# Optimization experiments

Hardware: AMD Instinct MI355X
Metric: run time of the kernel (lower is better)

The kernel has to match this reference:

```python
import jax, jax.numpy as jnp
import numpy as np
from jax import lax

HEADS = 4
DSTATE = 8
DHALF = 64
DTRANK = 8
GRID_SIZE = 5
SPLINE_ORDER = 3


def _ln(x, g, b, eps=1e-5):
    mu = x.mean(-1, keepdims=True)
    v = ((x - mu) ** 2).mean(-1, keepdims=True)
    return (x - mu) / jnp.sqrt(v + eps) * g + b


def _make_grid(in_f):
    h = 2.0 / GRID_SIZE
    g = jnp.arange(-SPLINE_ORDER, GRID_SIZE + SPLINE_ORDER + 1, dtype=jnp.float32) * h - 1.0
    return jnp.tile(g[None, :], (in_f, 1))  # (in, grid+2k+1)


def _b_splines(x, grid):
    # x: (batch, in); grid: (in, G+2k+1) -> (batch, in, G+k)
    xe = x[:, :, None]
    bases = ((xe >= grid[:, :-1]) & (xe < grid[:, 1:])).astype(x.dtype)
    for k in range(1, SPLINE_ORDER + 1):
        bases = ((xe - grid[:, :-(k + 1)]) / (grid[:, k:-1] - grid[:, :-(k + 1)])) * bases[:, :, :-1] \
              + ((grid[:, k + 1:] - xe) / (grid[:, k + 1:] - grid[:, 1:-k])) * bases[:, :, 1:]
    return bases


def _kan_layer(x, bw, sw, sc, grid):
    base = jax.nn.silu(x) @ bw.T
    bs = _b_splines(x, grid)
    return base + jnp.einsum('bic,oic->bo', bs, sw * sc[:, :, None])


def _fkan(x, ng, nb, bw0, sw0, sc0, bw1, sw1, sc1):
    B, N, C = x.shape
    xf = _ln(x, ng, nb).reshape(B * N, C)
    h = _kan_layer(xf, bw0, sw0, sc0, _make_grid(C))
    y = _kan_layer(h, bw1, sw1, sc1, _make_grid(bw0.shape[0]))
    return y.reshape(B, N, C)


def _conv1x1(x, w, b):
    return jnp.einsum('bchw,oc->bohw', x, w[:, :, 0, 0]) + b[None, :, None, None]


def _dwconv2d(x, w, b):
    y = lax.conv_general_dilated(x, w, (1, 1), 'SAME', feature_group_count=x.shape[1],
                                 dimension_numbers=('NCHW', 'OIHW', 'NCHW'))
    return y + b[None, :, None, None]


def _dwconv1d(x, w):
    return lax.conv_general_dilated(x, w, (1,), 'SAME', feature_group_count=x.shape[1],
                                    dimension_numbers=('NCH', 'OIH', 'NCH'))


def _attention(x, temp, qkv_w, qkv_b, dw_w, dw_b, po_w, po_b):
    b, c, h, w = x.shape
    qkv = _dwconv2d(_conv1x1(x, qkv_w, qkv_b), dw_w, dw_b)
    q, k, v = jnp.split(qkv, 3, axis=1)
    rs = lambda t: t.reshape(b, HEADS, c // HEADS, h * w)
    q, k, v = rs(q), rs(k), rs(v)
    q = q / jnp.maximum(jnp.linalg.norm(q, axis=-1, keepdims=True), 1e-12)
    k = k / jnp.maximum(jnp.linalg.norm(k, axis=-1, keepdims=True), 1e-12)
    attn = jax.nn.softmax(jnp.einsum('bhcn,bhdn->bhcd', q, k) * temp, axis=-1)
    out = jnp.einsum('bhcd,bhdn->bhcn', attn, v).reshape(b, c, h, w)
    return _conv1x1(out, po_w, po_b)


def _mamba(x, in_w, xp_w, dt_w, dt_b, A_log, Dp, out_w, cx_w, cz_w):
    B, L, C = x.shape
    xz = x @ in_w.T                       # (B, L, d_inner)
    xc, zc = jnp.split(xz, 2, axis=-1)    # each (B, L, DHALF)
    xl = jax.nn.silu(_dwconv1d(xc.transpose(0, 2, 1), cx_w)).transpose(0, 2, 1)
    zl = jax.nn.silu(_dwconv1d(zc.transpose(0, 2, 1), cz_w)).transpose(0, 2, 1)
    x_dbl = xl @ xp_w.T                   # (B, L, dt_rank + 2*d_state)
    dt, Bm, Cm = jnp.split(x_dbl, [DTRANK, DTRANK + DSTATE], axis=-1)
    delta = jax.nn.softplus(dt @ dt_w.T + dt_b)   # (B, L, DHALF)
    A = -jnp.exp(A_log)                   # (DHALF, DSTATE)
    dA = jnp.exp(jnp.einsum('bld,dn->bldn', delta, A))
    dBu = delta[..., None] * Bm[:, :, None, :] * xl[..., None]

    def step(hst, inp):
        dA_t, dBu_t, C_t = inp
        hst = dA_t * hst + dBu_t
        return hst, jnp.einsum('bdn,bn->bd', hst, C_t)

    h0 = jnp.zeros((B, DHALF, DSTATE), x.dtype)
    _, ys = lax.scan(step, h0, (dA.transpose(1, 0, 2, 3), dBu.transpose(1, 0, 2, 3), Cm.transpose(1, 0, 2)))
    y = ys.transpose(1, 0, 2) + xl * Dp
    return jnp.concatenate([y, zl], axis=-1) @ out_w.T


def _forward(x5d, ln1_g, ln1_b, ln2_g, ln2_b, ln3_g, ln3_b, ln4_g, ln4_b,
             attn_temp, attn_qkv_w, attn_qkv_b, attn_dw_w, attn_dw_b, attn_po_w, attn_po_b,
             ffn1_ng, ffn1_nb, ffn1_bw0, ffn1_sw0, ffn1_sc0, ffn1_bw1, ffn1_sw1, ffn1_sc1,
             ffn2_ng, ffn2_nb, ffn2_bw0, ffn2_sw0, ffn2_sc0, ffn2_bw1, ffn2_sw1, ffn2_sc1,
             in_proj_w, x_proj_w, dt_proj_w, dt_proj_b, A_log, D_param, out_proj_w, conv_x_w, conv_z_w):
    B, C, Dd, H, W = x5d.shape
    N = Dd * H * W
    Hs = int(np.sqrt(N))
    x = x5d.reshape(B, C, N).transpose(0, 2, 1)   # (B, N, C)
    t2d = _ln(x, ln1_g, ln1_b).transpose(0, 2, 1).reshape(B, C, Hs, Hs)
    a = _attention(t2d, attn_temp, attn_qkv_w, attn_qkv_b, attn_dw_w, attn_dw_b, attn_po_w, attn_po_b)
    t = x + a.reshape(B, C, N).transpose(0, 2, 1)
    u = _fkan(_ln(t, ln2_g, ln2_b), ffn1_ng, ffn1_nb, ffn1_bw0, ffn1_sw0, ffn1_sc0, ffn1_bw1, ffn1_sw1, ffn1_sc1) + t
    x_tr = x + u
    m = _mamba(_ln(x_tr, ln3_g, ln3_b), in_proj_w, x_proj_w, dt_proj_w, dt_proj_b, A_log, D_param, out_proj_w, conv_x_w, conv_z_w) + x_tr
    n = _fkan(_ln(m, ln4_g, ln4_b), ffn2_ng, ffn2_nb, ffn2_bw0, ffn2_sw0, ffn2_sc0, ffn2_bw1, ffn2_sw1, ffn2_sc1) + m
    out = x_tr + n
    return out.transpose(0, 2, 1).reshape(B, C, Dd, H, W)


def setup_inputs():
    key = jax.random.key(0)
    ks = iter(jax.random.split(key, 48))
    f32 = jnp.float32

    def rn(shape, s=0.05):
        return jax.random.normal(next(ks), shape, f32) * s

    B, C, Dd, H, W = 2, 128, 1, 96, 96
    MLP = 512
    d = {}
    d['x5d'] = jax.random.normal(next(ks), (B, C, Dd, H, W), f32)
    for nm in ('ln1', 'ln2', 'ln3', 'ln4'):
        d[nm + '_g'] = jnp.ones((C,), f32)
        d[nm + '_b'] = jnp.zeros((C,), f32)
    d['attn_temp'] = jnp.ones((HEADS, 1, 1), f32)
    d['attn_qkv_w'] = rn((3 * C, C, 1, 1)); d['attn_qkv_b'] = jnp.zeros((3 * C,), f32)
    d['attn_dw_w'] = rn((3 * C, 1, 3, 3), 0.2); d['attn_dw_b'] = jnp.zeros((3 * C,), f32)
    d['attn_po_w'] = rn((C, C, 1, 1)); d['attn_po_b'] = jnp.zeros((C,), f32)
    for p in ('ffn1', 'ffn2'):
        d[p + '_ng'] = jnp.ones((C,), f32); d[p + '_nb'] = jnp.zeros((C,), f32)
        d[p + '_bw0'] = rn((MLP, C)); d[p + '_sw0'] = rn((MLP, C, GRID_SIZE + SPLINE_ORDER), 0.02); d[p + '_sc0'] = jnp.ones((MLP, C), f32)
        d[p + '_bw1'] = rn((C, MLP)); d[p + '_sw1'] = rn((C, MLP, GRID_SIZE + SPLINE_ORDER), 0.02); d[p + '_sc1'] = jnp.ones((C, MLP), f32)
    d['in_proj_w'] = rn((C, C))
    d['x_proj_w'] = rn((DTRANK + 2 * DSTATE, DHALF))
    std = DTRANK ** -0.5
    d['dt_proj_w'] = jax.random.uniform(next(ks), (DHALF, DTRANK), f32, -std, std)
    dt = jnp.exp(jax.random.uniform(next(ks), (DHALF,), f32) * (np.log(0.1) - np.log(0.001)) + np.log(0.001))
    dt = jnp.clip(dt, 1e-4, None)
    d['dt_proj_b'] = dt + jnp.log(-jnp.expm1(-dt))
    d['A_log'] = jnp.log(jnp.tile(jnp.arange(1, DSTATE + 1, dtype=f32)[None, :], (DHALF, 1)))
    d['D_param'] = jnp.ones((DHALF,), f32)
    d['out_proj_w'] = rn((C, C))
    d['conv_x_w'] = rn((DHALF, 1, 3), 0.2)
    d['conv_z_w'] = rn((DHALF, 1, 3), 0.2)
    return d


def reference(x5d, ln1_g, ln1_b, ln2_g, ln2_b, ln3_g, ln3_b, ln4_g, ln4_b,
              attn_temp, attn_qkv_w, attn_qkv_b, attn_dw_w, attn_dw_b, attn_po_w, attn_po_b,
              ffn1_ng, ffn1_nb, ffn1_bw0, ffn1_sw0, ffn1_sc0, ffn1_bw1, ffn1_sw1, ffn1_sc1,
              ffn2_ng, ffn2_nb, ffn2_bw0, ffn2_sw0, ffn2_sc0, ffn2_bw1, ffn2_sw1, ffn2_sc1,
              in_proj_w, x_proj_w, dt_proj_w, dt_proj_b, A_log, D_param, out_proj_w, conv_x_w, conv_z_w):
    return _forward(x5d, ln1_g, ln1_b, ln2_g, ln2_b, ln3_g, ln3_b, ln4_g, ln4_b,
                    attn_temp, attn_qkv_w, attn_qkv_b, attn_dw_w, attn_dw_b, attn_po_w, attn_po_b,
                    ffn1_ng, ffn1_nb, ffn1_bw0, ffn1_sw0, ffn1_sc0, ffn1_bw1, ffn1_sw1, ffn1_sc1,
                    ffn2_ng, ffn2_nb, ffn2_bw0, ffn2_sw0, ffn2_sc0, ffn2_bw1, ffn2_sw1, ffn2_sc1,
                    in_proj_w, x_proj_w, dt_proj_w, dt_proj_b, A_log, D_param, out_proj_w, conv_x_w, conv_z_w)
```

## Files before the change

### kernel.cpp

```cpp
#include <hip/hip_runtime.h>

typedef unsigned short u16;
typedef __attribute__((ext_vector_type(8))) short bh8;
typedef __attribute__((ext_vector_type(4))) float f4;

#define DI __device__ __forceinline__

DI u16 f2bf(float f){ unsigned u=__float_as_uint(f); u += 0x7fffu + ((u>>16)&1u); return (u16)(u>>16); }
DI float bf2f(u16 u){ return __uint_as_float(((unsigned)u)<<16); }
DI float silu_f(float x){ return x/(1.f+__expf(-x)); }

DI void gld16(const u16* g, u16* l){
  __builtin_amdgcn_global_load_lds((const __attribute__((address_space(1))) void*)g,
                                   (__attribute__((address_space(3))) void*)l, 16, 0, 0);
}

DI void bspline8(float x, float* v){
  float u = x*2.5f + 5.5f;
  #pragma unroll
  for (int j=0;j<8;j++){
    float a  = fabsf(u - (float)(j+2));
    float t1 = fmaxf(2.f-a, 0.f);
    float t2 = fmaxf(1.f-a, 0.f);
    v[j] = t1*t1*t1*(1.f/6.f) - t2*t2*t2*(2.f/3.f);
  }
}

template<int KAN_H, bool OUT_BF16>
__global__ __launch_bounds__(256, 4)
void gemm64(const void* __restrict__ Asrc, const u16* __restrict__ Bt,
            void* __restrict__ Cout, int M, int N, int K, int ktiles_per_z,
            int split, const float* __restrict__ bias, const float* __restrict__ R1)
{
  __shared__ u16 sA[64*64 + 8];
  __shared__ u16 sB[128*64];
  const int m0 = blockIdx.y * 64;
  const int n0 = blockIdx.x * 128;
  const int ktiles = K >> 6;
  int kt0 = blockIdx.z * ktiles_per_z;
  int kt1 = kt0 + ktiles_per_z; if (kt1 > ktiles) kt1 = ktiles;
  const int t = threadIdx.x;
  const int wave = t >> 6, lane = t & 63;
  const int lr = lane & 15, lq = lane >> 4;
  const int lr8 = lane >> 3, lc8 = lane & 7;
  const int swz8 = lc8 ^ lr8;
  f4 acc[4][2];
  f4 z4 = {0.f,0.f,0.f,0.f};
  #pragma unroll
  for (int i=0;i<4;i++){ acc[i][0]=z4; acc[i][1]=z4; }

  for (int kt = kt0; kt < kt1; ++kt) {
    int k0 = kt << 6;
    {
      const u16* Bp = Bt + (size_t)n0 * K + k0;
      #pragma unroll
      for (int it=0; it<4; ++it) {
        int r = it*32 + wave*8;
        gld16(Bp + (size_t)(r + lr8) * K + swz8*8, &sB[r*64]);
      }
    }
    if (KAN_H == 0) {
      const u16* Ap = (const u16*)Asrc + (size_t)m0 * K + k0;
      #pragma unroll
      for (int it=0; it<2; ++it) {
        int r = it*32 + wave*8;
        gld16(Ap + (size_t)(r + lr8) * K + swz8*8, &sA[r*64]);
      }
    } else {
      const u16* hsrc = (const u16*)Asrc;
      if (k0 < KAN_H) {
        #pragma unroll
        for (int it=0; it<2; ++it) {
          int chunk = t + it*256;
          int r = chunk >> 3, ck = chunk & 7;
          const u16* src = hsrc + (size_t)(m0+r)*KAN_H + k0 + ck*8;
          ushort4 a = *(const ushort4*)src;
          ushort4 b2 = *(const ushort4*)(src+4);
          alignas(16) u16 o[8];
          o[0]=f2bf(silu_f(bf2f(a.x))); o[1]=f2bf(silu_f(bf2f(a.y)));
          o[2]=f2bf(silu_f(bf2f(a.z))); o[3]=f2bf(silu_f(bf2f(a.w)));
          o[4]=f2bf(silu_f(bf2f(b2.x))); o[5]=f2bf(silu_f(bf2f(b2.y)));
          o[6]=f2bf(silu_f(bf2f(b2.z))); o[7]=f2bf(silu_f(bf2f(b2.w)));
          *(float4*)(&sA[r*64 + (ck ^ (r&7))*8]) = *(const float4*)o;
        }
      } else {
        int i0 = (k0 - KAN_H) >> 3;
        const float4 zf4 = make_float4(0.f,0.f,0.f,0.f);
        #pragma unroll
        for (int it=0; it<2; ++it) {
          int pair = t + it*256;
          int r = pair >> 3, ii = pair & 7;
          int base = r*64 + (ii ^ (r&7))*8;
          *(float4*)(&sA[base]) = zf4;
          float x = bf2f(hsrc[(size_t)(m0+r)*KAN_H + i0 + ii]);
          float u = x*2.5f + 5.5f;
          bool valid = (u >= 0.f) & (u < 11.f);
          float uc = fminf(fmaxf(u, 0.f), 10.999f);
          int m = (int)uc;
          float tt = uc - (float)m;
          float omt = 1.f - tt, t2 = tt*tt, t3 = t2*tt;
          float w0 = omt*omt*omt*(1.f/6.f);
          float w3 = t3*(1.f/6.f);
          float w1 = 0.5f*t3 - t2 + (2.f/3.f);
          float w2 = 1.f - w0 - w1 - w3;
          float ws[4] = {w0, w1, w2, w3};
          int c0 = m - 3;
          #pragma unroll
          for (int j=0;j<4;j++){
            int c = c0 + j;
            bool ok = valid & ((unsigned)c < 8u);
            int off = ok ? (base + c) : (64*64);
            sA[off] = f2bf(ws[j]);
          }
        }
      }
    }
    __syncthreads();
    #pragma unroll
    for (int kk=0; kk<64; kk+=32) {
      const int c0k = kk >> 3;
      bh8 af[4], bfr[2];
      #pragma unroll
      for (int i=0;i<4;i++) {
        int row = i*16 + lr;
        af[i] = *(const bh8*)(&sA[row*64 + ((c0k+lq) ^ (row&7))*8]);
      }
      #pragma unroll
      for (int j=0;j<2;j++) {
        int row = wave*32 + j*16 + lr;
        bfr[j] = *(const bh8*)(&sB[row*64 + ((c0k+lq) ^ (row&7))*8]);
      }
      #pragma unroll
      for (int i=0;i<4;i++)
        #pragma unroll
        for (int j=0;j<2;j++)
          acc[i][j] = __builtin_amdgcn_mfma_f32_16x16x32_bf16(af[i], bfr[j], acc[i][j], 0, 0, 0);
    }
    __syncthreads();
  }
  float* Cf = (float*)Cout;
  if (!OUT_BF16 && split) Cf += (size_t)blockIdx.z * M * N;
  u16* Cb = (u16*)Cout;
  #pragma unroll
  for (int i=0;i<4;i++) {
    int row = m0 + i*16 + lq*4;
    #pragma unroll
    for (int j=0;j<2;j++) {
      int col = n0 + wave*32 + j*16 + lr;
      float bv = bias ? bias[col] : 0.f;
      #pragma unroll
      for (int r4=0;r4<4;r4++) {
        size_t idx = (size_t)(row + r4) * N + col;
        float v = acc[i][j][r4] + bv;
        if (OUT_BF16) {
          Cb[idx] = f2bf(v);
        } else {
          if (R1) v += R1[idx];
          Cf[idx] = v;
        }
      }
    }
  }
}

__global__ __launch_bounds__(256) void k_ln1_trans(const float* __restrict__ x5d,
    float* __restrict__ x_t, u16* __restrict__ ln1_t,
    const float* __restrict__ g, const float* __restrict__ bv)
{
  __shared__ float tile[128*65];
  __shared__ float red_s[256], red_q[256];
  __shared__ float st_mu[64], st_rs[64];
  int b = blockIdx.y, n0 = blockIdx.x * 64;
  int j = threadIdx.x & 63, part = threadIdx.x >> 6;
  for (int cc=0; cc<32; ++cc) {
    int c = part*32 + cc;
    tile[c*65 + j] = x5d[((size_t)b*128 + c)*9216 + n0 + j];
  }
  __syncthreads();
  float s=0.f, s2=0.f;
  for (int cc=0; cc<32; ++cc) {
    float v = tile[(part*32+cc)*65 + j];
    s += v; s2 += v*v;
  }
  red_s[threadIdx.x]=s; red_q[threadIdx.x]=s2;
  __syncthreads();
  if (threadIdx.x < 64) {
    int jj = threadIdx.x;
    float ts = red_s[jj]+red_s[jj+64]+red_s[jj+128]+red_s[jj+192];
    float tq = red_q[jj]+red_q[jj+64]+red_q[jj+128]+red_q[jj+192];
    float mu = ts*(1.f/128.f);
    st_mu[jj]=mu;
    st_rs[jj]=rsqrtf(tq*(1.f/128.f) - mu*mu + 1e-5f);
  }
  __syncthreads();
  for (int it=0; it<32; ++it) {
    int idx = threadIdx.x + it*256;
    int tok = idx >> 7, c = idx & 127;
    float v = tile[c*65 + tok];
    size_t a = ((size_t)b*9216 + n0 + tok)*128 + c;
    x_t[a] = v;
    ln1_t[a] = f2bf((v - st_mu[tok])*st_rs[tok]*g[c] + bv[c]);
  }
}

__global__ void k_ln_double_expand(const float* __restrict__ in, u16* __restrict__ A1,
    const float* __restrict__ g1, const float* __restrict__ b1,
    const float* __restrict__ g2, const float* __restrict__ b2)
{
  int tok = blockIdx.x*4 + (threadIdx.x>>6);
  int lane = threadIdx.x & 63;
  const float* row = in + (size_t)tok*128;
  float v0=row[lane], v1=row[lane+64];
  float s=v0+v1, s2=v0*v0+v1*v1;
  #pragma unroll
  for (int o=1;o<64;o<<=1){ s += __shfl_xor(s,o); s2 += __shfl_xor(s2,o); }
  float mu=s*(1.f/128.f);
  float rs=rsqrtf(s2*(1.f/128.f)-mu*mu+1e-5f);
  float y0=(v0-mu)*rs*g1[lane]+b1[lane];
  float y1=(v1-mu)*rs*g1[lane+64]+b1[lane+64];
  s=y0+y1; s2=y0*y0+y1*y1;
  #pragma unroll
  for (int o=1;o<64;o<<=1){ s += __shfl_xor(s,o); s2 += __shfl_xor(s2,o); }
  mu=s*(1.f/128.f);
  rs=rsqrtf(s2*(1.f/128.f)-mu*mu+1e-5f);
  y0=(y0-mu)*rs*g2[lane]+b2[lane];
  y1=(y1-mu)*rs*g2[lane+64]+b2[lane+64];
  u16* arow = A1 + (size_t)tok*1152;
  arow[lane]    = f2bf(silu_f(y0));
  arow[lane+64] = f2bf(silu_f(y1));
  float w[8]; alignas(16) u16 o8[8];
  bspline8(y0, w);
  #pragma unroll
  for (int j=0;j<8;j++) o8[j]=f2bf(w[j]);
  *(float4*)(&arow[128 + lane*8]) = *(const float4*)o8;
  bspline8(y1, w);
  #pragma unroll
  for (int j=0;j<8;j++) o8[j]=f2bf(w[j]);
  *(float4*)(&arow[128 + (lane+64)*8]) = *(const float4*)o8;
}

__global__ __launch_bounds__(256) void k_dwconv(const u16* __restrict__ qkv_t,
    u16* __restrict__ qkvd, const float* __restrict__ dw_w, const float* __restrict__ dw_b)
{
  __shared__ float lt[100*68];
  int tile = blockIdx.x; int th=(tile/12)*8, tw=(tile%12)*8;
  int cg = blockIdx.y, b = blockIdx.z;
  int t = threadIdx.x;
  for (int pp=0; pp<7; ++pp) {
    int pos = pp*16 + (t>>4);
    if (pos < 100) {
      int ih = th + pos/10 - 1, iw = tw + pos%10 - 1;
      int c4 = (t & 15)*4;
      float4 v = make_float4(0.f,0.f,0.f,0.f);
      if (ih>=0 && ih<96 && iw>=0 && iw<96) {
        ushort4 raw = *(const ushort4*)&qkv_t[(((size_t)b*9216) + ih*96 + iw)*384 + cg*64 + c4];
        v = make_float4(bf2f(raw.x), bf2f(raw.y), bf2f(raw.z), bf2f(raw.w));
      }
      *(float4*)&lt[pos*68 + c4] = v;
    }
  }
  __syncthreads();
  int ch = t & 63, gch = cg*64 + ch;
  float w[9];
  #pragma unroll
  for (int k=0;k<9;k++) w[k]=dw_w[gch*9+k];
  float bias = dw_b[gch];
  for (int pp=0; pp<16; ++pp) {
    int pos = (t>>6) + pp*4;
    int oh = pos>>3, ow = pos&7;
    float acc = bias;
    #pragma unroll
    for (int di=0; di<3; ++di)
      #pragma unroll
      for (int dj=0; dj<3; ++dj)
        acc += lt[((oh+di)*10 + ow+dj)*68 + ch] * w[di*3+dj];
    qkvd[(((size_t)b*9216) + (th+oh)*96 + tw+ow)*384 + gch] = f2bf(acc);
  }
}

__global__ void k_normsum(const u16* __restrict__ qkvd, float* __restrict__ ss)
{
  int b = blockIdx.y, n0 = blockIdx.x*128;
  int c = threadIdx.x;
  float acc=0.f;
  for (int i=0;i<128;++i){
    float v = bf2f(qkvd[((size_t)b*9216 + n0+i)*384 + c]);
    acc += v*v;
  }
  atomicAdd(&ss[b*256 + c], acc);
}

__global__ __launch_bounds__(256) void k_qk(const u16* __restrict__ qkvd,
    const float* __restrict__ ss, float* __restrict__ S)
{
  __shared__ float ql[128][32];
  __shared__ float kl[128][32];
  int nc=blockIdx.x, h=blockIdx.y, b=blockIdx.z;
  int t = threadIdx.x;
  int r = t>>1, half = t&1;
  size_t rowa = ((size_t)b*9216 + nc*128 + r)*384 + (half?128:0) + h*32;
  #pragma unroll
  for (int cc=0; cc<32; ++cc) {
    float v = bf2f(qkvd[rowa + cc]);
    if (half) kl[r][cc]=v; else ql[r][cc]=v;
  }
  __syncthreads();
  int i0 = (t>>4)*2, j0 = (t&15)*2;
  float a00=0.f,a01=0.f,a10=0.f,a11=0.f;
  for (int n=0;n<128;++n){
    float2 qv = *(const float2*)&ql[n][i0];
    float2 kv = *(const float2*)&kl[n][j0];
    a00 += qv.x*kv.x; a01 += qv.x*kv.y;
    a10 += qv.y*kv.x; a11 += qv.y*kv.y;
  }
  const float* ssb = ss + b*256;
  float rq0 = 1.f/fmaxf(sqrtf(ssb[h*32+i0]),1e-12f);
  float rq1 = 1.f/fmaxf(sqrtf(ssb[h*32+i0+1]),1e-12f);
  float rk0 = 1.f/fmaxf(sqrtf(ssb[128+h*32+j0]),1e-12f);
  float rk1 = 1.f/fmaxf(sqrtf(ssb[128+h*32+j0+1]),1e-12f);
  float* Sp = S + ((size_t)(b*4+h))*1024;
  atomicAdd(&Sp[i0*32+j0],     a00*rq0*rk0);
  atomicAdd(&Sp[i0*32+j0+1],   a01*rq0*rk1);
  atomicAdd(&Sp[(i0+1)*32+j0], a10*rq1*rk0);
  atomicAdd(&Sp[(i0+1)*32+j0+1], a11*rq1*rk1);
}

__global__ void k_softmax(const float* __restrict__ S, float* __restrict__ attnP,
                          const float* __restrict__ temp)
{
  int bh = blockIdx.x; int h = bh & 3;
  int i = threadIdx.x;
  const float* row = S + (size_t)bh*1024 + i*32;
  float tp = temp[h];
  float vals[32]; float mx = -1e30f;
  #pragma unroll
  for (int j=0;j<32;++j){ float v=row[j]*tp; vals[j]=v; mx=fmaxf(mx,v); }
  float sum=0.f;
  #pragma unroll
  for (int j=0;j<32;++j){ vals[j]=__expf(vals[j]-mx); sum+=vals[j]; }
  float inv=1.f/sum;
  float* out = attnP + (size_t)bh*1024 + i*32;
  #pragma unroll
  for (int j=0;j<32;++j) out[j]=vals[j]*inv;
}

__global__ __launch_bounds__(256) void k_av(const u16* __restrict__ qkvd,
    const float* __restrict__ attnP, u16* __restrict__ attnout)
{
  __shared__ float at[1024];
  int b=blockIdx.z, h=blockIdx.y;
  int n = blockIdx.x*256 + threadIdx.x;
  #pragma unroll
  for (int it=0;it<4;++it)
    at[threadIdx.x + it*256] = attnP[((size_t)(b*4+h))*1024 + threadIdx.x + it*256];
  __syncthreads();
  const u16* vrow = &qkvd[((size_t)b*9216 + n)*384 + 256 + h*32];
  float acc[32];
  #pragma unroll
  for (int i=0;i<32;++i) acc[i]=0.f;
  #pragma unroll 4
  for (int j=0;j<32;++j){
    float vj = bf2f(vrow[j]);
    #pragma unroll
    for (int i=0;i<32;++i) acc[i] += at[i*32+j]*vj;
  }
  u16* orow = &attnout[((size_t)b*9216 + n)*128 + h*32];
  #pragma unroll
  for (int i=0;i<32;++i) orow[i] = f2bf(acc[i]);
}

__global__ void k_reduce4(const float4* __restrict__ P, const float4* __restrict__ R1,
                          const float4* __restrict__ R2, float4* __restrict__ o, int n4)
{
  int i = blockIdx.x*256 + threadIdx.x;
  if (i<n4){
    float4 a=P[i], b=P[i+n4], c=P[i+2*n4], d=P[i+3*n4], r=R1[i], s=R2[i];
    o[i]=make_float4(a.x+b.x+c.x+d.x+r.x+s.x, a.y+b.y+c.y+d.y+r.y+s.y,
                     a.z+b.z+c.z+d.z+r.z+s.z, a.w+b.w+c.w+d.w+r.w+s.w);
  }
}

__global__ void k_reduce4_ln(const float4* __restrict__ P, const float4* __restrict__ R1,
    const float4* __restrict__ R2, float4* __restrict__ xtr, u16* __restrict__ xm,
    const float* __restrict__ g, const float* __restrict__ bv, int n4)
{
  int i = blockIdx.x*256 + threadIdx.x;
  int q = i & 31;
  float4 a=P[i], b=P[i+n4], c=P[i+2*n4], d=P[i+3*n4], r=R1[i], s=R2[i];
  float4 v=make_float4(a.x+b.x+c.x+d.x+r.x+s.x, a.y+b.y+c.y+d.y+r.y+s.y,
                       a.z+b.z+c.z+d.z+r.z+s.z, a.w+b.w+c.w+d.w+r.w+s.w);
  xtr[i]=v;
  float s1 = v.x+v.y+v.z+v.w;
  float s2 = v.x*v.x+v.y*v.y+v.z*v.z+v.w*v.w;
  #pragma unroll
  for (int o=1;o<32;o<<=1){ s1 += __shfl_xor(s1,o); s2 += __shfl_xor(s2,o); }
  float mu = s1*(1.f/128.f);
  float rs = rsqrtf(s2*(1.f/128.f)-mu*mu+1e-5f);
  float4 g4 = *(const float4*)(g + q*4);
  float4 b4 = *(const float4*)(bv + q*4);
  ushort4 o4;
  o4.x = f2bf((v.x-mu)*rs*g4.x + b4.x);
  o4.y = f2bf((v.y-mu)*rs*g4.y + b4.y);
  o4.z = f2bf((v.z-mu)*rs*g4.z + b4.z);
  o4.w = f2bf((v.w-mu)*rs*g4.w + b4.w);
  ((ushort4*)xm)[i] = o4;
}

__global__ void k_prep(const float* __restrict__ qkv_w, const float* __restrict__ po_w,
    const float* __restrict__ in_w, const float* __restrict__ out_w,
    const float* __restrict__ A_log, u16* __restrict__ qkvw_bf, u16* __restrict__ pow_bf,
    u16* __restrict__ inw_bf, u16* __restrict__ outw_bf, float* __restrict__ Aneg,
    float* __restrict__ zbuf, int nz)
{
  int i = blockIdx.x*256 + threadIdx.x;
  if (i < 49152) { qkvw_bf[i] = f2bf(qkv_w[i]); return; }
  i -= 49152;
  if (i < 16384) { pow_bf[i] = f2bf(po_w[i]); return; }
  i -= 16384;
  if (i < 16384) { inw_bf[i] = f2bf(in_w[i]); return; }
  i -= 16384;
  if (i < 16384) { outw_bf[i] = f2bf(out_w[i]); return; }
  i -= 16384;
  if (i < 512) { Aneg[i] = -__expf(A_log[i]); return; }
  i -= 512;
  if (i < nz) zbuf[i] = 0.f;
}

__global__ __launch_bounds__(256) void k_mamba_pre(const float* __restrict__ xz,
    float* __restrict__ xl, float* __restrict__ delta,
    float* __restrict__ Bm, float* __restrict__ Cm, u16* __restrict__ A_out,
    const float* __restrict__ cxw, const float* __restrict__ czw,
    const float* __restrict__ xpw, const float* __restrict__ dtw, const float* __restrict__ dtb)
{
  __shared__ float xls[4][64];
  __shared__ float xds[4][24];
  int w = threadIdx.x>>6;
  int tok = blockIdx.x*4 + w;
  int lane = threadIdx.x & 63;
  int l = tok % 9216;
  size_t base = (size_t)tok*128;
  float xm1 = (l>0)?     xz[base-128+lane]    : 0.f;
  float x0  =            xz[base+lane];
  float xp1 = (l<9215)?  xz[base+128+lane]    : 0.f;
  float zm1 = (l>0)?     xz[base-128+64+lane] : 0.f;
  float z0  =            xz[base+64+lane];
  float zp1 = (l<9215)?  xz[base+128+64+lane] : 0.f;
  float xc = silu_f(cxw[lane*3]*xm1 + cxw[lane*3+1]*x0 + cxw[lane*3+2]*xp1);
  float zc = silu_f(czw[lane*3]*zm1 + czw[lane*3+1]*z0 + czw[lane*3+2]*zp1);
  xl[(size_t)tok*64+lane] = xc;
  A_out[(size_t)tok*128 + 64 + lane] = f2bf(zc);
  xls[w][lane] = xc;
  __syncthreads();
  if (lane < 24) {
    float s=0.f;
    #pragma unroll 8
    for (int c=0;c<64;++c) s += xls[w][c]*xpw[lane*64+c];
    xds[w][lane]=s;
  }
  __syncthreads();
  float dacc = dtb[lane];
  #pragma unroll
  for (int r=0;r<8;++r) dacc += xds[w][r]*dtw[lane*8+r];
  delta[(size_t)tok*64+lane] = (dacc>20.f)? dacc : log1pf(__expf(dacc));
  if (lane<8)       Bm[(size_t)tok*8+lane]   = xds[w][8+lane];
  else if (lane<16) Cm[(size_t)tok*8+lane-8] = xds[w][16+lane-8];
}

__global__ __launch_bounds__(512) void k_scan1(const float* __restrict__ delta,
    const float* __restrict__ Bm, const float* __restrict__ xl,
    const float* __restrict__ Aneg, float* __restrict__ cP, float* __restrict__ cS)
{
  int b=blockIdx.y, ch=blockIdx.x;
  int t=threadIdx.x; int d=t>>3, n=t&7;
  float An = Aneg[d*8+n];
  float P=1.f, S=0.f;
  int l0 = ch*96;
  #pragma unroll 8
  for (int i=0;i<96;++i){
    size_t s = (size_t)b*9216 + l0+i;
    float del = delta[s*64+d];
    float a = __expf(del*An);
    float dbu = del * Bm[s*8+n] * xl[s*64+d];
    P *= a; S = fmaf(a,S,dbu);
  }
  size_t o = ((size_t)(b*96+ch))*512 + t;
  cP[o]=P; cS[o]=S;
}

__global__ __launch_bounds__(512) void k_scan2(const float* __restrict__ cP,
    const float* __restrict__ cS, float* __restrict__ cI)
{
  int b=blockIdx.x; int t=threadIdx.x;
  float carry=0.f;
  #pragma unroll 4
  for (int c=0;c<96;++c){
    size_t o = ((size_t)(b*96+c))*512 + t;
    cI[o]=carry;
    carry = fmaf(cP[o], carry, cS[o]);
  }
}

__global__ __launch_bounds__(512) void k_scan3(const float* __restrict__ delta,
    const float* __restrict__ Bm, const float* __restrict__ Cm,
    const float* __restrict__ xl, const float* __restrict__ Aneg,
    const float* __restrict__ Dp, const float* __restrict__ cI, u16* __restrict__ A_out)
{
  int b=blockIdx.y, ch=blockIdx.x;
  int t=threadIdx.x; int d=t>>3, n=t&7;
  float An = Aneg[d*8+n];
  float h = cI[((size_t)(b*96+ch))*512 + t];
  float Dd = Dp[d];
  int l0 = ch*96;
  #pragma unroll 4
  for (int i=0;i<96;++i){
    size_t s = (size_t)b*9216 + l0+i;
    float del = delta[s*64+d];
    float a = __expf(del*An);
    float xv = xl[s*64+d];
    h = fmaf(a, h, del * Bm[s*8+n] * xv);
    float contrib = h * Cm[s*8+n];
    contrib += __shfl_xor(contrib,1);
    contrib += __shfl_xor(contrib,2);
    contrib += __shfl_xor(contrib,4);
    if (n==0) A_out[s*128 + d] = f2bf(contrib + xv*Dd);
  }
}

__global__ __launch_bounds__(256) void k_transpose_out(const float* __restrict__ sfin,
                                                       float* __restrict__ out)
{
  __shared__ float tile[128*65];
  int b=blockIdx.y, n0=blockIdx.x*64;
  for (int it=0;it<32;++it){
    int idx = threadIdx.x + it*256;
    int tok = idx>>7, c = idx&127;
    tile[c*65+tok] = sfin[((size_t)b*9216 + n0+tok)*128 + c];
  }
  __syncthreads();
  int j = threadIdx.x & 63, part = threadIdx.x>>6;
  for (int cc=0;cc<32;++cc){
    int c = part*32+cc;
    out[((size_t)b*128 + c)*9216 + n0 + j] = tile[c*65 + j];
  }
}

__global__ void k_pack_w1t(const float* __restrict__ bw0, const float* __restrict__ sw0,
                           const float* __restrict__ sc0, u16* __restrict__ W1t)
{
  int idx = blockIdx.x*256 + threadIdx.x;
  if (idx >= 512*1152) return;
  int o = idx/1152, k = idx%1152;
  float v;
  if (k < 128) v = bw0[o*128+k];
  else { int i=(k-128)>>3, c=(k-128)&7; v = sw0[(o*128+i)*8+c]*sc0[o*128+i]; }
  W1t[idx]=f2bf(v);
}
__global__ void k_pack_w2t(const float* __restrict__ bw1, const float* __restrict__ sw1,
                           const float* __restrict__ sc1, u16* __restrict__ W2t)
{
  int idx = blockIdx.x*256 + threadIdx.x;
  if (idx >= 128*4608) return;
  int o = idx/4608, k = idx%4608;
  float v;
  if (k < 512) v = bw1[o*512+k];
  else { int i=(k-512)>>3, c=(k-512)&7; v = sw1[(o*512+i)*8+c]*sc1[o*512+i]; }
  W2t[idx]=f2bf(v);
}

extern "C" void kernel_launch(void* const* d_in, const int* in_sizes, int n_in,
                              void* d_out, int out_size, void* d_ws, size_t ws_size,
                              hipStream_t stream)
{
  (void)in_sizes; (void)n_in; (void)out_size; (void)ws_size;
  const float* x5d   =(const float*)d_in[0];
  const float* ln1_g =(const float*)d_in[1];
  const float* ln1_b =(const float*)d_in[2];
  const float* ln2_g =(const float*)d_in[3];
  const float* ln2_b =(const float*)d_in[4];
  const float* ln3_g =(const float*)d_in[5];
  const float* ln3_b =(const float*)d_in[6];
  const float* ln4_g =(const float*)d_in[7];
  const float* ln4_b =(const float*)d_in[8];
  const float* temp  =(const float*)d_in[9];
  const float* qkv_w =(const float*)d_in[10];
  const float* qkv_b =(const float*)d_in[11];
  const float* dw_w  =(const float*)d_in[12];
  const float* dw_b  =(const float*)d_in[13];
  const float* po_w  =(const float*)d_in[14];
  const float* po_b  =(const float*)d_in[15];
  const float* f1_ng =(const float*)d_in[16];
  const float* f1_nb =(const float*)d_in[17];
  const float* f1_bw0=(const float*)d_in[18];
  const float* f1_sw0=(const float*)d_in[19];
  const float* f1_sc0=(const float*)d_in[20];
  const float* f1_bw1=(const float*)d_in[21];
  const float* f1_sw1=(const float*)d_in[22];
  const float* f1_sc1=(const float*)d_in[23];
  const float* f2_ng =(const float*)d_in[24];
  const float* f2_nb =(const float*)d_in[25];
  const float* f2_bw0=(const float*)d_in[26];
  const float* f2_sw0=(const float*)d_in[27];
  const float* f2_sc0=(const float*)d_in[28];
  const float* f2_bw1=(const float*)d_in[29];
  const float* f2_sw1=(const float*)d_in[30];
  const float* f2_sc1=(const float*)d_in[31];
  const float* in_w  =(const float*)d_in[32];
  const float* xp_w  =(const float*)d_in[33];
  const float* dt_w  =(const float*)d_in[34];
  const float* dt_b  =(const float*)d_in[35];
  const float* A_log =(const float*)d_in[36];
  const float* Dp    =(const float*)d_in[37];
  const float* out_w =(const float*)d_in[38];
  const float* cx_w  =(const float*)d_in[39];
  const float* cz_w  =(const float*)d_in[40];
  float* out = (float*)d_out;

  const size_t T = 18432;
  char* wsb = (char*)d_ws;
  size_t off = 0;
  auto alloc = [&](size_t bytes)->void* {
    void* p = wsb + off; off += (bytes + 255) & ~(size_t)255; return p;
  };
  float* x_t    = (float*)alloc(T*128*4);
  char*  scrA   = (char*) alloc(38*1024*1024);
  float* ssS    = (float*)alloc((512+8192+8192)*4);
  float* t_t    = (float*)alloc(T*128*4);
  u16*   A1     = (u16*)  alloc(T*1152*2);
  u16*   hbuf   = (u16*)  alloc(T*512*2);
  float* xtr    = (float*)alloc(T*128*4);
  u16*   xm     = (u16*)  alloc(T*128*2);
  float* xl     = (float*)alloc(T*64*4);
  float* delta  = (float*)alloc(T*64*4);
  float* Bm     = (float*)alloc(T*8*4);
  float* Cm     = (float*)alloc(T*8*4);
  u16*   A_out  = (u16*)  alloc(T*128*2);
  float* cP     = (float*)alloc(2*96*512*4);
  float* cS     = (float*)alloc(2*96*512*4);
  float* cI     = (float*)alloc(2*96*512*4);
  float* sfin   = (float*)alloc(T*128*4);
  u16* qkvw_bf  = (u16*)alloc(384*128*2);
  u16* pow_bf   = (u16*)alloc(128*128*2);
  u16* inw_bf   = (u16*)alloc(128*128*2);
  u16* outw_bf  = (u16*)alloc(128*128*2);
  u16* W1t_a    = (u16*)alloc(512*1152*2);
  u16* W2t_a    = (u16*)alloc(128*4608*2);
  u16* W1t_b    = (u16*)alloc(512*1152*2);
  u16* W2t_b    = (u16*)alloc(128*4608*2);
  float* Aneg   = (float*)alloc(512*4);
  float* ss = ssS;
  float* S  = ssS + 512;
  float* attnP = ssS + 512 + 8192;
  u16*   ln1_t  = (u16*)(scrA);
  u16*   qkv_tb = (u16*)(scrA + 4718592);
  u16*   qkvd   = (u16*)(scrA + 4718592 + 14155776);
  u16*   attnout= (u16*)(scrA + 4718592 + 2*14155776);
  float* part   = (float*)scrA;
  float* xz     = (float*)scrA;
  float* m_t    = t_t;

  k_pack_w1t<<<2304,256,0,stream>>>(f1_bw0, f1_sw0, f1_sc0, W1t_a);
  k_pack_w1t<<<2304,256,0,stream>>>(f2_bw0, f2_sw0, f2_sc0, W1t_b);
  k_pack_w2t<<<2304,256,0,stream>>>(f1_bw1, f1_sw1, f1_sc1, W2t_a);
  k_pack_w2t<<<2304,256,0,stream>>>(f2_bw1, f2_sw1, f2_sc1, W2t_b);
  k_prep<<<420,256,0,stream>>>(qkv_w, po_w, in_w, out_w, A_log,
      qkvw_bf, pow_bf, inw_bf, outw_bf, Aneg, ssS, 512+8192);

  k_ln1_trans<<<dim3(144,2),256,0,stream>>>(x5d, x_t, ln1_t, ln1_g, ln1_b);
  gemm64<0,true><<<dim3(3,288,1),256,0,stream>>>(ln1_t, qkvw_bf, qkv_tb,
      18432, 384, 128, 2, 0, qkv_b, nullptr);
  k_dwconv<<<dim3(144,6,2),256,0,stream>>>(qkv_tb, qkvd, dw_w, dw_b);
  k_normsum<<<dim3(72,2),256,0,stream>>>(qkvd, ss);
  k_qk<<<dim3(72,4,2),256,0,stream>>>(qkvd, ss, S);
  k_softmax<<<8,32,0,stream>>>(S, attnP, temp);
  k_av<<<dim3(36,4,2),256,0,stream>>>(qkvd, attnP, attnout);
  gemm64<0,false><<<dim3(1,288,1),256,0,stream>>>(attnout, pow_bf, t_t,
      18432, 128, 128, 2, 0, po_b, x_t);

  k_ln_double_expand<<<4608,256,0,stream>>>(t_t, A1, ln2_g, ln2_b, f1_ng, f1_nb);
  gemm64<0,true><<<dim3(4,288,1),256,0,stream>>>(A1, W1t_a, hbuf,
      18432, 512, 1152, 18, 0, nullptr, nullptr);
  gemm64<512,false><<<dim3(1,288,4),256,0,stream>>>(hbuf, W2t_a, part,
      18432, 128, 4608, 18, 1, nullptr, nullptr);
  k_reduce4_ln<<<2304,256,0,stream>>>((const float4*)part, (const float4*)t_t,
      (const float4*)x_t, (float4*)xtr, xm, ln3_g, ln3_b, (int)(T*128/4));

  gemm64<0,false><<<dim3(1,288,1),256,0,stream>>>(xm, inw_bf, xz,
      18432, 128, 128, 2, 0, nullptr, nullptr);
  k_mamba_pre<<<4608,256,0,stream>>>(xz, xl, delta, Bm, Cm, A_out,
      cx_w, cz_w, xp_w, dt_w, dt_b);
  k_scan1<<<dim3(96,2),512,0,stream>>>(delta, Bm, xl, Aneg, cP, cS);
  k_scan2<<<2,512,0,stream>>>(cP, cS, cI);
  k_scan3<<<dim3(96,2),512,0,stream>>>(delta, Bm, Cm, xl, Aneg, Dp, cI, A_out);
  gemm64<0,false><<<dim3(1,288,1),256,0,stream>>>(A_out, outw_bf, m_t,
      18432, 128, 128, 2, 0, nullptr, xtr);

  k_ln_double_expand<<<4608,256,0,stream>>>(m_t, A1, ln4_g, ln4_b, f2_ng, f2_nb);
  gemm64<0,true><<<dim3(4,288,1),256,0,stream>>>(A1, W1t_b, hbuf,
      18432, 512, 1152, 18, 0, nullptr, nullptr);
  gemm64<512,false><<<dim3(1,288,4),256,0,stream>>>(hbuf, W2t_b, part,
      18432, 128, 4608, 18, 1, nullptr, nullptr);
  k_reduce4<<<2304,256,0,stream>>>((const float4*)part, (const float4*)m_t,
      (const float4*)xtr, (float4*)sfin, (int)(T*128/4));

  k_transpose_out<<<dim3(144,2),256,0,stream>>>(sfin, out);
}
```

Measured before the change: 530.4 us.

## Use two-wave GEMM blocks with larger per-wave tiles and LDS-staged bf16 stores

The GEMM kernel drops from four waves to two waves per 64x128 block, so each wave computes a 64x64 output sub-tile with a 4x4 MFMA accumulator grid instead of 4x2. Each A fragment loaded from LDS is now reused over more MFMAs, which cuts LDS reads per MFMA. The bf16 output path now goes through shared memory and is written with 16-byte coalesced stores instead of scattered 2-byte stores. In exchange, register pressure roughly doubles and the block holds fewer threads, which may lower occupancy and latency hiding.

```diff
diff --git a/kernel.cpp b/kernel.cpp
--- a/kernel.cpp
+++ b/kernel.cpp
@@ -27,13 +27,14 @@
 }
 
 template<int KAN_H, bool OUT_BF16>
-__global__ __launch_bounds__(256, 4)
-void gemm64(const void* __restrict__ Asrc, const u16* __restrict__ Bt,
+__global__ __launch_bounds__(128, 3)
+void gemm2w(const void* __restrict__ Asrc, const u16* __restrict__ Bt,
             void* __restrict__ Cout, int M, int N, int K, int ktiles_per_z,
             int split, const float* __restrict__ bias, const float* __restrict__ R1)
 {
-  __shared__ u16 sA[64*64 + 8];
-  __shared__ u16 sB[128*64];
+  __shared__ __align__(128) u16 smem[12304];
+  u16* const sB = smem;
+  u16* const sA = smem + 8192;
   const int m0 = blockIdx.y * 64;
   const int n0 = blockIdx.x * 128;
   const int ktiles = K >> 6;
@@ -44,34 +45,36 @@
   const int lr = lane & 15, lq = lane >> 4;
   const int lr8 = lane >> 3, lc8 = lane & 7;
   const int swz8 = lc8 ^ lr8;
-  f4 acc[4][2];
+  f4 acc[4][4];
   f4 z4 = {0.f,0.f,0.f,0.f};
   #pragma unroll
-  for (int i=0;i<4;i++){ acc[i][0]=z4; acc[i][1]=z4; }
+  for (int i=0;i<4;i++)
+    #pragma unroll
+    for (int j=0;j<4;j++) acc[i][j]=z4;
 
   for (int kt = kt0; kt < kt1; ++kt) {
     int k0 = kt << 6;
     {
       const u16* Bp = Bt + (size_t)n0 * K + k0;
       #pragma unroll
-      for (int it=0; it<4; ++it) {
-        int r = it*32 + wave*8;
+      for (int it=0; it<8; ++it) {
+        int r = it*16 + wave*8;
         gld16(Bp + (size_t)(r + lr8) * K + swz8*8, &sB[r*64]);
       }
     }
     if (KAN_H == 0) {
       const u16* Ap = (const u16*)Asrc + (size_t)m0 * K + k0;
       #pragma unroll
-      for (int it=0; it<2; ++it) {
-        int r = it*32 + wave*8;
+      for (int it=0; it<4; ++it) {
+        int r = it*16 + wave*8;
         gld16(Ap + (size_t)(r + lr8) * K + swz8*8, &sA[r*64]);
       }
     } else {
       const u16* hsrc = (const u16*)Asrc;
       if (k0 < KAN_H) {
         #pragma unroll
-        for (int it=0; it<2; ++it) {
-          int chunk = t + it*256;
+        for (int it=0; it<4; ++it) {
+          int chunk = t + it*128;
           int r = chunk >> 3, ck = chunk & 7;
           const u16* src = hsrc + (size_t)(m0+r)*KAN_H + k0 + ck*8;
           ushort4 a = *(const ushort4*)src;
@@ -87,8 +90,8 @@
         int i0 = (k0 - KAN_H) >> 3;
         const float4 zf4 = make_float4(0.f,0.f,0.f,0.f);
         #pragma unroll
-        for (int it=0; it<2; ++it) {
-          int pair = t + it*256;
+        for (int it=0; it<4; ++it) {
+          int pair = t + it*128;
           int r = pair >> 3, ii = pair & 7;
           int base = r*64 + (ii ^ (r&7))*8;
           *(float4*)(&sA[base]) = zf4;
@@ -109,7 +112,7 @@
           for (int j=0;j<4;j++){
             int c = c0 + j;
             bool ok = valid & ((unsigned)c < 8u);
-            int off = ok ? (base + c) : (64*64);
+            int off = ok ? (base + c) : 4096;
             sA[off] = f2bf(ws[j]);
           }
         }
@@ -119,42 +122,62 @@
     #pragma unroll
     for (int kk=0; kk<64; kk+=32) {
       const int c0k = kk >> 3;
-      bh8 af[4], bfr[2];
+      bh8 af[4], bfr[4];
       #pragma unroll
       for (int i=0;i<4;i++) {
         int row = i*16 + lr;
         af[i] = *(const bh8*)(&sA[row*64 + ((c0k+lq) ^ (row&7))*8]);
       }
       #pragma unroll
-      for (int j=0;j<2;j++) {
-        int row = wave*32 + j*16 + lr;
+      for (int j=0;j<4;j++) {
+        int row = wave*64 + j*16 + lr;
         bfr[j] = *(const bh8*)(&sB[row*64 + ((c0k+lq) ^ (row&7))*8]);
       }
       #pragma unroll
       for (int i=0;i<4;i++)
         #pragma unroll
-        for (int j=0;j<2;j++)
+        for (int j=0;j<4;j++)
           acc[i][j] = __builtin_amdgcn_mfma_f32_16x16x32_bf16(af[i], bfr[j], acc[i][j], 0, 0, 0);
     }
     __syncthreads();
   }
-  float* Cf = (float*)Cout;
-  if (!OUT_BF16 && split) Cf += (size_t)blockIdx.z * M * N;
-  u16* Cb = (u16*)Cout;
-  #pragma unroll
-  for (int i=0;i<4;i++) {
-    int row = m0 + i*16 + lq*4;
+  if (OUT_BF16) {
+    u16* Cb = (u16*)Cout;
     #pragma unroll
-    for (int j=0;j<2;j++) {
-      int col = n0 + wave*32 + j*16 + lr;
-      float bv = bias ? bias[col] : 0.f;
+    for (int i=0;i<4;i++) {
       #pragma unroll
-      for (int r4=0;r4<4;r4++) {
-        size_t idx = (size_t)(row + r4) * N + col;
-        float v = acc[i][j][r4] + bv;
-        if (OUT_BF16) {
-          Cb[idx] = f2bf(v);
-        } else {
+      for (int j=0;j<4;j++) {
+        int col = wave*64 + j*16 + lr;
+        float bv = bias ? bias[n0 + col] : 0.f;
+        #pragma unroll
+        for (int r4=0;r4<4;r4++) {
+          int row = i*16 + lq*4 + r4;
+          smem[row*136 + col] = f2bf(acc[i][j][r4] + bv);
+        }
+      }
+    }
+    __syncthreads();
+    #pragma unroll
+    for (int it=0; it<8; ++it) {
+      int idx = t + it*128;
+      int row = idx >> 4, seg = idx & 15;
+      *(float4*)(Cb + (size_t)(m0+row)*N + n0 + seg*8) =
+          *(const float4*)&smem[row*136 + seg*8];
+    }
+  } else {
+    float* Cf = (float*)Cout;
+    if (split) Cf += (size_t)blockIdx.z * M * N;
+    #pragma unroll
+    for (int i=0;i<4;i++) {
+      int row = m0 + i*16 + lq*4;
+      #pragma unroll
+      for (int j=0;j<4;j++) {
+        int col = n0 + wave*64 + j*16 + lr;
+        float bv = bias ? bias[col] : 0.f;
+        #pragma unroll
+        for (int r4=0;r4<4;r4++) {
+          size_t idx = (size_t)(row + r4) * N + col;
+          float v = acc[i][j][r4] + bv;
           if (R1) v += R1[idx];
           Cf[idx] = v;
         }
@@ -666,38 +689,38 @@
       qkvw_bf, pow_bf, inw_bf, outw_bf, Aneg, ssS, 512+8192);
 
   k_ln1_trans<<<dim3(144,2),256,0,stream>>>(x5d, x_t, ln1_t, ln1_g, ln1_b);
-  gemm64<0,true><<<dim3(3,288,1),256,0,stream>>>(ln1_t, qkvw_bf, qkv_tb,
+  gemm2w<0,true><<<dim3(3,288,1),128,0,stream>>>(ln1_t, qkvw_bf, qkv_tb,
       18432, 384, 128, 2, 0, qkv_b, nullptr);
   k_dwconv<<<dim3(144,6,2),256,0,stream>>>(qkv_tb, qkvd, dw_w, dw_b);
   k_normsum<<<dim3(72,2),256,0,stream>>>(qkvd, ss);
   k_qk<<<dim3(72,4,2),256,0,stream>>>(qkvd, ss, S);
   k_softmax<<<8,32,0,stream>>>(S, attnP, temp);
   k_av<<<dim3(36,4,2),256,0,stream>>>(qkvd, attnP, attnout);
-  gemm64<0,false><<<dim3(1,288,1),256,0,stream>>>(attnout, pow_bf, t_t,
+  gemm2w<0,false><<<dim3(1,288,1),128,0,stream>>>(attnout, pow_bf, t_t,
       18432, 128, 128, 2, 0, po_b, x_t);
 
   k_ln_double_expand<<<4608,256,0,stream>>>(t_t, A1, ln2_g, ln2_b, f1_ng, f1_nb);
-  gemm64<0,true><<<dim3(4,288,1),256,0,stream>>>(A1, W1t_a, hbuf,
+  gemm2w<0,true><<<dim3(4,288,1),128,0,stream>>>(A1, W1t_a, hbuf,
       18432, 512, 1152, 18, 0, nullptr, nullptr);
-  gemm64<512,false><<<dim3(1,288,4),256,0,stream>>>(hbuf, W2t_a, part,
+  gemm2w<512,false><<<dim3(1,288,4),128,0,stream>>>(hbuf, W2t_a, part,
       18432, 128, 4608, 18, 1, nullptr, nullptr);
   k_reduce4_ln<<<2304,256,0,stream>>>((const float4*)part, (const float4*)t_t,
       (const float4*)x_t, (float4*)xtr, xm, ln3_g, ln3_b, (int)(T*128/4));
 
-  gemm64<0,false><<<dim3(1,288,1),256,0,stream>>>(xm, inw_bf, xz,
+  gemm2w<0,false><<<dim3(1,288,1),128,0,stream>>>(xm, inw_bf, xz,
       18432, 128, 128, 2, 0, nullptr, nullptr);
   k_mamba_pre<<<4608,256,0,stream>>>(xz, xl, delta, Bm, Cm, A_out,
       cx_w, cz_w, xp_w, dt_w, dt_b);
   k_scan1<<<dim3(96,2),512,0,stream>>>(delta, Bm, xl, Aneg, cP, cS);
   k_scan2<<<2,512,0,stream>>>(cP, cS, cI);
   k_scan3<<<dim3(96,2),512,0,stream>>>(delta, Bm, Cm, xl, Aneg, Dp, cI, A_out);
-  gemm64<0,false><<<dim3(1,288,1),256,0,stream>>>(A_out, outw_bf, m_t,
+  gemm2w<0,false><<<dim3(1,288,1),128,0,stream>>>(A_out, outw_bf, m_t,
       18432, 128, 128, 2, 0, nullptr, xtr);
 
   k_ln_double_expand<<<4608,256,0,stream>>>(m_t, A1, ln4_g, ln4_b, f2_ng, f2_nb);
-  gemm64<0,true><<<dim3(4,288,1),256,0,stream>>>(A1, W1t_b, hbuf,
+  gemm2w<0,true><<<dim3(4,288,1),128,0,stream>>>(A1, W1t_b, hbuf,
       18432, 512, 1152, 18, 0, nullptr, nullptr);
-  gemm64<512,false><<<dim3(1,288,4),256,0,stream>>>(hbuf, W2t_b, part,
+  gemm2w<512,false><<<dim3(1,288,4),128,0,stream>>>(hbuf, W2t_b, part,
       18432, 128, 4608, 18, 1, nullptr, nullptr);
   k_reduce4<<<2304,256,0,stream>>>((const float4*)part, (const float4*)m_t,
       (const float4*)xtr, (float4*)sfin, (int)(T*128/4));
```

After: 563.6 us. +6.3%, slower.
